# Kernel tuning notes

Hardware: AMD Instinct MI355X
Metric: run time of the kernel (lower is better)

Reference implementation:

```python
import jax, jax.numpy as jnp
import numpy as np

T, N, E = 4, 4096, 65536
XD, HD, ZD = 256, 256, 64
EPS = 1e-10


def setup_inputs() -> dict:
    key = jax.random.key(0)
    ks = jax.random.split(key, 30)
    rn = lambda k, sh, s=0.05: jax.random.normal(k, sh, dtype=jnp.float32) * s
    inp = {
        "x": rn(ks[0], (T, N, XD), 1.0),
        "edge_idx": jax.random.randint(ks[1], (T, 2, E), 0, N, dtype=jnp.int32),
        "adj": jax.random.bernoulli(ks[2], 0.005, (T, N, N)).astype(jnp.float32),
        "eps_noise": jax.random.normal(ks[3], (T, N, ZD), dtype=jnp.float32),
        "h0": jnp.zeros((1, N, HD), jnp.float32),
        # phi_x / phi_z (Linear+ReLU)
        "phi_x_w": rn(ks[4], (XD, HD)), "phi_x_b": jnp.zeros((HD,), jnp.float32),
        "phi_z_w": rn(ks[5], (ZD, HD)), "phi_z_b": jnp.zeros((HD,), jnp.float32),
        # encoder GCNs
        "enc_w": rn(ks[6], (2 * HD, HD)), "enc_b": jnp.zeros((HD,), jnp.float32),
        "enc_mean_w": rn(ks[7], (HD, ZD)), "enc_mean_b": jnp.zeros((ZD,), jnp.float32),
        "enc_std_w": rn(ks[8], (HD, ZD)), "enc_std_b": jnp.zeros((ZD,), jnp.float32),
        # prior MLPs
        "prior_w": rn(ks[9], (HD, HD)), "prior_b": jnp.zeros((HD,), jnp.float32),
        "prior_mean_w": rn(ks[10], (HD, ZD)), "prior_mean_b": jnp.zeros((ZD,), jnp.float32),
        "prior_std_w": rn(ks[11], (HD, ZD)), "prior_std_b": jnp.zeros((ZD,), jnp.float32),
        # graph-GRU GCNs (bias=False, n_layers=1; x-input is cat[phi_x, phi_z] -> 2*HD)
        "gru_xz_w": rn(ks[12], (2 * HD, HD)), "gru_hz_w": rn(ks[13], (HD, HD)),
        "gru_xr_w": rn(ks[14], (2 * HD, HD)), "gru_hr_w": rn(ks[15], (HD, HD)),
        "gru_xh_w": rn(ks[16], (2 * HD, HD)), "gru_hh_w": rn(ks[17], (HD, HD)),
    }
    return inp


def _gcn(xf, src, dst, W, b):
    """GCNConv: sym-normalized (A + I) aggregation, then bias. Returns pre-activation."""
    h = xf @ W                                             # [N, out]
    deg = 1.0 + jax.ops.segment_sum(jnp.ones(src.shape[0], xf.dtype), dst, num_segments=N)
    dinv = jax.lax.rsqrt(deg)                              # [N]
    norm = dinv[src] * dinv[dst]                           # [E]
    agg = jax.ops.segment_sum(h[src] * norm[:, None], dst, num_segments=N)
    agg = agg + (dinv * dinv)[:, None] * h                 # self-loop term
    if b is not None:
        agg = agg + b
    return agg


def reference(x, edge_idx, adj, eps_noise, h0,
              phi_x_w, phi_x_b, phi_z_w, phi_z_b,
              enc_w, enc_b, enc_mean_w, enc_mean_b, enc_std_w, enc_std_b,
              prior_w, prior_b, prior_mean_w, prior_mean_b, prior_std_w, prior_std_b,
              gru_xz_w, gru_hz_w, gru_xr_w, gru_hr_w, gru_xh_w, gru_hh_w):
    relu, sp, sig = jax.nn.relu, jax.nn.softplus, jax.nn.sigmoid
    h = h0                                                  # [1, N, HD]
    kld = jnp.float32(0.0)
    nll = jnp.float32(0.0)
    enc_means, prior_means = [], []
    nn_f = jnp.float32(N * N)
    for t in range(T):
        src, dst = edge_idx[t, 0], edge_idx[t, 1]
        phi_x_t = relu(x[t] @ phi_x_w + phi_x_b)                       # [N, HD]
        enc_in = jnp.concatenate([phi_x_t, h[-1]], axis=1)             # [N, 2HD]
        enc_t = relu(_gcn(enc_in, src, dst, enc_w, enc_b))
        enc_mean_t = _gcn(enc_t, src, dst, enc_mean_w, enc_mean_b)     # act = identity
        enc_std_t = sp(_gcn(enc_t, src, dst, enc_std_w, enc_std_b))
        prior_t = relu(h[-1] @ prior_w + prior_b)
        prior_mean_t = prior_t @ prior_mean_w + prior_mean_b
        prior_std_t = sp(prior_t @ prior_std_w + prior_std_b)
        z_t = eps_noise[t] * enc_std_t + enc_mean_t                    # reparameterize
        phi_z_t = relu(z_t @ phi_z_w + phi_z_b)
        dec_t = sig(z_t @ z_t.T)                                       # [N, N] decode
        # graph-GRU step (n_layers = 1, bias=False)
        gin = jnp.concatenate([phi_x_t, phi_z_t], axis=1)              # [N, 2HD]
        z_g = sig(_gcn(gin, src, dst, gru_xz_w, None) + _gcn(h[0], src, dst, gru_hz_w, None))
        r_g = sig(_gcn(gin, src, dst, gru_xr_w, None) + _gcn(h[0], src, dst, gru_hr_w, None))
        h_tilde = jnp.tanh(_gcn(gin, src, dst, gru_xh_w, None)
                           + _gcn(r_g * h[0], src, dst, gru_hh_w, None))
        h = (z_g * h[0] + (1.0 - z_g) * h_tilde)[None]                 # [1, N, HD]
        # KLD (faithful to _kld_gauss, including its sign convention)
        s1, s2 = enc_std_t + EPS, prior_std_t + EPS
        kld_el = (2.0 * jnp.log(s2) - 2.0 * jnp.log(s1)
                  - (s1 * s1 + (enc_mean_t - prior_mean_t) ** 2) / (s2 * s2) + 1.0)
        kld = kld + (0.5 / N) * jnp.mean(jnp.sum(kld_el, axis=0))
        # NLL (faithful quirk: BCE-with-logits applied to sigmoid output dec_t)
        a = adj[t]
        tsum = jnp.sum(a)
        posw = (nn_f - tsum) / tsum
        norm = nn_f / ((nn_f - tsum) * 2.0)
        bce = posw * a * sp(-dec_t) + (1.0 - a) * sp(dec_t)
        nll = nll + norm * jnp.mean(bce)
        enc_means.append(enc_mean_t)
        prior_means.append(prior_mean_t)
    return kld, nll, jnp.stack(enc_means), jnp.stack(prior_means), h
```

## Files before the change

### kernel.cpp

```cpp
#include <hip/hip_runtime.h>
#include <hip/hip_bf16.h>

#define T_STEPS 4
#define N 4096
#define E 65536
#define XD 256
#define HD 256
#define ZD 64

typedef __hip_bfloat16 bf16;
typedef __attribute__((ext_vector_type(8))) short short8;
typedef __attribute__((ext_vector_type(4))) float f32x4;

__device__ __forceinline__ float b2f(bf16 v){ return __bfloat162float(v); }
__device__ __forceinline__ bf16 f2b(float v){ return __float2bfloat16(v); }
__device__ __forceinline__ short f2s(float v){ return __builtin_bit_cast(short, f2b(v)); }
__device__ __forceinline__ float bits2f(unsigned int s){ return __builtin_bit_cast(float, s << 16); }
__device__ __forceinline__ float s2f(short s){ return bits2f((unsigned int)(unsigned short)s); }
__device__ __forceinline__ float splus(float x){ return (x > 20.f) ? x : log1pf(expf(x)); }
__device__ __forceinline__ float sigm(float x){ return 1.f/(1.f + expf(-x)); }

__device__ __forceinline__ float ldI(const void* p, size_t i, int f){
  return f ? ((const float*)p)[i] : b2f(((const bf16*)p)[i]);
}
__device__ __forceinline__ void stO(void* p, size_t i, float v, int f){
  if (f) ((float*)p)[i] = v; else ((bf16*)p)[i] = f2b(v);
}
__device__ __forceinline__ void ld8b(const bf16* p, float v[8]){
  uint4 u = *(const uint4*)p;
  v[0]=bits2f(u.x & 0xffffu); v[1]=bits2f(u.x >> 16);
  v[2]=bits2f(u.y & 0xffffu); v[3]=bits2f(u.y >> 16);
  v[4]=bits2f(u.z & 0xffffu); v[5]=bits2f(u.z >> 16);
  v[6]=bits2f(u.w & 0xffffu); v[7]=bits2f(u.w >> 16);
}
__device__ __forceinline__ unsigned int pack2(float a, float b){
  return (unsigned int)(unsigned short)__builtin_bit_cast(unsigned short, f2b(a))
       | ((unsigned int)(unsigned short)__builtin_bit_cast(unsigned short, f2b(b)) << 16);
}

union SMem {
  struct { short As[64*40]; short Wt[64*40]; } g;
  struct { short Zi[64*72]; short Zj[64*72]; short Adj[64*72]; float red[256]; } z;
  struct { float msh[16*128]; } m;
  int sh[256];
  float red[256];
};

struct KP {
  const void *x, *adj, *eps, *h0;
  const int* ei;
  const void *phi_x_w, *phi_x_b, *phi_z_w, *phi_z_b;
  const void *enc_w, *enc_b, *enc_mean_w, *enc_mean_b, *enc_std_w, *enc_std_b;
  const void *prior_w, *prior_b, *prior_mean_w, *prior_mean_b, *prior_std_w, *prior_std_b;
  const void *gxz, *ghz, *gxr, *ghr, *gxh, *ghh;
  void* out;
  float* scal; int* dflag; float* dinv; int* offs; int* srcs; float* enorm; int* deg;
  float* h_prev; bf16* h_bf; bf16* phiXa; bf16* Tb1; bf16* Tb2;
  bf16* zbf; float* z_g; bf16* Gs1; bf16* Gsx; bf16* Gms; bf16* Gh2;
};

#define OUT_EM ((size_t)2)
#define OUT_PM ((size_t)(2 + (size_t)T_STEPS*N*ZD))
#define OUT_H  ((size_t)(2 + (size_t)2*T_STEPS*N*ZD))

__device__ void mfma_tile(SMem& sm, int tid, int f,
    const void* A1, int am1, int lda1, const void* A2, int am2, int lda2,
    int K1, int K, const void* W, int ldw, int wcol,
    const void* bias, int act, bf16* C, int ldc, int row0, int ccol0){
  int ar = tid >> 2, akk = (tid & 3)*8;
  int wk = tid >> 3, wn = (tid & 7)*8;
  int wave = tid >> 6, lane = tid & 63, m = lane & 15, kq = lane >> 4;
  f32x4 acc[4] = {};
  for (int k0 = 0; k0 < K; k0 += 32){
    const void* A; int am, lda, kb;
    if (k0 < K1){ A = A1; am = am1; lda = lda1; kb = k0; }
    else        { A = A2; am = am2; lda = lda2; kb = k0 - K1; }
    size_t aidx = (size_t)(row0 + ar)*lda + kb + akk;
    short8 av;
    if (am == 2 || (am == 1 && f == 0)){
      av = *(const short8*)((const short*)A + aidx);
    } else {
      const float* Af = (const float*)A;
      float4 u0 = *(const float4*)(Af + aidx);
      float4 u1 = *(const float4*)(Af + aidx + 4);
      av[0]=f2s(u0.x); av[1]=f2s(u0.y); av[2]=f2s(u0.z); av[3]=f2s(u0.w);
      av[4]=f2s(u1.x); av[5]=f2s(u1.y); av[6]=f2s(u1.z); av[7]=f2s(u1.w);
    }
    *(short8*)&sm.g.As[ar*40 + akk] = av;
    size_t wi = (size_t)(k0 + wk)*ldw + wcol + wn;
    short wv[8];
    if (f == 0){
      short8 t8 = *(const short8*)((const short*)W + wi);
      #pragma unroll
      for (int j = 0; j < 8; j++) wv[j] = t8[j];
    } else {
      const float* Wf = (const float*)W;
      float4 u0 = *(const float4*)(Wf + wi);
      float4 u1 = *(const float4*)(Wf + wi + 4);
      wv[0]=f2s(u0.x); wv[1]=f2s(u0.y); wv[2]=f2s(u0.z); wv[3]=f2s(u0.w);
      wv[4]=f2s(u1.x); wv[5]=f2s(u1.y); wv[6]=f2s(u1.z); wv[7]=f2s(u1.w);
    }
    #pragma unroll
    for (int j = 0; j < 8; j++){
      int nrow = wn + j;
      int col = (((wk >> 3) ^ ((nrow >> 3) & 3)) << 3) | (wk & 7);
      sm.g.Wt[nrow*40 + col] = wv[j];
    }
    __syncthreads();
    short8 afr = *(const short8*)&sm.g.As[(wave*16 + m)*40 + kq*8];
    #pragma unroll
    for (int t4 = 0; t4 < 4; t4++){
      int nb = t4*16 + m;
      short8 bfr = *(const short8*)&sm.g.Wt[nb*40 + ((kq ^ ((nb >> 3) & 3)) << 3)];
      acc[t4] = __builtin_amdgcn_mfma_f32_16x16x32_bf16(afr, bfr, acc[t4], 0, 0, 0);
    }
    __syncthreads();
  }
  #pragma unroll
  for (int t4 = 0; t4 < 4; t4++){
    int c = ccol0 + t4*16 + m;
    float bv = bias ? ldI(bias, wcol + t4*16 + m, f) : 0.f;
    #pragma unroll
    for (int reg = 0; reg < 4; reg++){
      int r = row0 + wave*16 + kq*4 + reg;
      float v = acc[t4][reg] + bv;
      if (act == 1) v = fmaxf(v, 0.f);
      C[(size_t)r*ldc + c] = f2b(v);
    }
  }
}

__device__ void dec_tile1(const KP& p, SMem& sm, int tid, int t, int u, int f){
  int i0 = (u >> 6)*64, j0 = (u & 63)*64;
  size_t aoff = (size_t)t*N*N;
  #pragma unroll
  for (int i = 0; i < 2; i++){
    int idx = tid + i*256;
    int r = idx >> 3, c = idx & 7;
    int col = ((c ^ ((r >> 3) & 3)) << 3);
    *(short8*)&sm.z.Zi[r*72 + col] = *(const short8*)((const short*)p.zbf + (size_t)(i0+r)*ZD + c*8);
    *(short8*)&sm.z.Zj[r*72 + col] = *(const short8*)((const short*)p.zbf + (size_t)(j0+r)*ZD + c*8);
  }
  {
    int row = tid >> 2, c0 = (tid & 3)*16;
    if (f){
      const float* ap = (const float*)p.adj + aoff + (size_t)(i0+row)*N + j0 + c0;
      short tmp[16];
      #pragma unroll
      for (int q = 0; q < 16; q += 4){
        float4 v = *(const float4*)(ap + q);
        tmp[q]=f2s(v.x); tmp[q+1]=f2s(v.y); tmp[q+2]=f2s(v.z); tmp[q+3]=f2s(v.w);
      }
      *(short8*)&sm.z.Adj[row*72 + c0]     = *(short8*)&tmp[0];
      *(short8*)&sm.z.Adj[row*72 + c0 + 8] = *(short8*)&tmp[8];
    } else {
      const short* ap = (const short*)p.adj + aoff + (size_t)(i0+row)*N + j0 + c0;
      *(short8*)&sm.z.Adj[row*72 + c0]     = *(const short8*)ap;
      *(short8*)&sm.z.Adj[row*72 + c0 + 8] = *(const short8*)(ap + 8);
    }
  }
  __syncthreads();
  int wave = tid >> 6, lane = tid & 63, m = lane & 15, kq = lane >> 4;
  int ra = wave*16 + m, sa = (ra >> 3) & 3;
  short8 a1 = *(const short8*)&sm.z.Zi[ra*72 + ((kq ^ sa) << 3)];
  short8 a2 = *(const short8*)&sm.z.Zi[ra*72 + (((kq+4) ^ sa) << 3)];
  f32x4 acc[4] = {};
  #pragma unroll
  for (int t4 = 0; t4 < 4; t4++){
    int rb = t4*16 + m, sb2 = (rb >> 3) & 3;
    short8 b1 = *(const short8*)&sm.z.Zj[rb*72 + ((kq ^ sb2) << 3)];
    short8 b2 = *(const short8*)&sm.z.Zj[rb*72 + (((kq+4) ^ sb2) << 3)];
    acc[t4] = __builtin_amdgcn_mfma_f32_16x16x32_bf16(a1, b1, acc[t4], 0, 0, 0);
    acc[t4] = __builtin_amdgcn_mfma_f32_16x16x32_bf16(a2, b2, acc[t4], 0, 0, 0);
  }
  float lts = 0.f, lP = 0.f, lQ = 0.f;
  #pragma unroll
  for (int t4 = 0; t4 < 4; t4++){
    int lj = t4*16 + m;
    #pragma unroll
    for (int reg = 0; reg < 4; reg++){
      int li = wave*16 + kq*4 + reg;
      float av = s2f(sm.z.Adj[li*72 + lj]);
      float dec = sigm(acc[t4][reg]);
      lts += av;
      lQ += (1.f - av)*log1pf(expf(dec));
      if (av != 0.f) lP += av*log1pf(expf(-dec));
    }
  }
  __syncthreads();
  sm.z.red[tid] = lts; __syncthreads();
  for (int o = 128; o > 0; o >>= 1){ if (tid < o) sm.z.red[tid] += sm.z.red[tid+o]; __syncthreads(); }
  if (tid == 0) atomicAdd(p.scal + 8 + t, sm.z.red[0]);
  __syncthreads();
  sm.z.red[tid] = lP; __syncthreads();
  for (int o = 128; o > 0; o >>= 1){ if (tid < o) sm.z.red[tid] += sm.z.red[tid+o]; __syncthreads(); }
  if (tid == 0) atomicAdd(p.scal + 12 + t, sm.z.red[0]);
  __syncthreads();
  sm.z.red[tid] = lQ; __syncthreads();
  for (int o = 128; o > 0; o >>= 1){ if (tid < o) sm.z.red[tid] += sm.z.red[tid+o]; __syncthreads(); }
  if (tid == 0) atomicAdd(p.scal + 16 + t, sm.z.red[0]);
}

__global__ __launch_bounds__(256) void setup0_k(KP p){
  int gb = blockIdx.x, tid = threadIdx.x;
  if (gb == 0){ if (tid < 64) p.scal[tid] = 0.f; }
  else if (gb == 1){
    if (tid == 0){
      const unsigned short* u = (const unsigned short*)p.x;
      int big = 0;
      for (int i = 0; i < 256; i++){ int e = (u[i] >> 7) & 0xFF; if (e >= 134) big++; }
      *p.dflag = (big > 16) ? 1 : 0;
    }
  } else {
    p.deg[(gb-2)*256 + tid] = 0;
  }
}

__global__ __launch_bounds__(256) void count_deg_k(KP p){
  int idx = blockIdx.x*256 + threadIdx.x;
  int t = idx >> 16, e = idx & (E-1);
  int dst = p.ei[(size_t)t*2*E + E + e] & (N-1);
  atomicAdd(&p.deg[t*N + dst], 1);
}

__global__ __launch_bounds__(256) void setup2_k(KP p){
  __shared__ SMem sm;
  int gb = blockIdx.x, tid = threadIdx.x;
  int f = *p.dflag;
  if (gb < 4){
    int t = gb;
    const int* dg = p.deg + t*N;
    int* of = p.offs + t*(N+1);
    int base = tid*16;
    int loc[16]; int s = 0;
    #pragma unroll
    for (int i = 0; i < 16; i++){ loc[i] = s; s += dg[base+i]; }
    sm.sh[tid] = s;
    __syncthreads();
    for (int o = 1; o < 256; o <<= 1){
      int v = (tid >= o) ? sm.sh[tid-o] : 0;
      __syncthreads();
      sm.sh[tid] += v;
      __syncthreads();
    }
    int pre = (tid == 0) ? 0 : sm.sh[tid-1];
    #pragma unroll
    for (int i = 0; i < 16; i++){
      int deg_i = dg[base+i];
      of[base+i] = pre + loc[i];
      p.dinv[t*N + base + i] = rsqrtf(1.f + (float)deg_i);
    }
    if (tid == 255) of[N] = sm.sh[255];
    __syncthreads();
    #pragma unroll
    for (int i = 0; i < 16; i++) p.deg[t*N + base + i] = pre + loc[i];
  } else if (gb < 36){
    for (int idx = (gb-4)*256 + tid; idx < N*HD; idx += 32*256){
      float v = ldI(p.h0, idx, f);
      p.h_prev[idx] = v; p.h_bf[idx] = f2b(v);
    }
  } else {
    for (int u = gb - 36; u < 1024; u += 988){
      int colblk = u & 3, rowblk = u >> 2;
      mfma_tile(sm, tid, f, p.x, 1, XD, nullptr, 0, 0, XD, XD,
                p.phi_x_w, HD, colblk*64, p.phi_x_b, 1,
                p.phiXa, HD, rowblk*64, colblk*64);
    }
  }
}

__global__ __launch_bounds__(256) void scatter_k(KP p){
  int idx = blockIdx.x*256 + threadIdx.x;
  int t = idx >> 16, e = idx & (E-1);
  int s = p.ei[(size_t)t*2*E + e] & (N-1);
  int d = p.ei[(size_t)t*2*E + E + e] & (N-1);
  int pos = atomicAdd(&p.deg[t*N + d], 1);
  if (pos >= 0 && pos < E){
    p.srcs[(size_t)t*E + pos] = s;
    p.enorm[(size_t)t*E + pos] = p.dinv[t*N + s] * p.dinv[t*N + d];
  }
}

__global__ __launch_bounds__(256) void g1_k(KP p, int t){
  __shared__ SMem sm;
  int gb = blockIdx.x, tid = threadIdx.x, f = *p.dflag;
  const bf16* phiX = p.phiXa + (size_t)t*N*HD;
  int colblk = gb & 15, rowblk = gb >> 4;
  int grp = colblk >> 2, c4 = colblk & 3;
  if (grp == 0)
    mfma_tile(sm, tid, f, phiX, 2, HD, p.h_bf, 2, HD, 256, 512,
              p.enc_w, HD, c4*64, nullptr, 0, p.Gs1, 1024, rowblk*64, colblk*64);
  else if (grp == 1)
    mfma_tile(sm, tid, f, p.h_bf, 2, HD, nullptr, 0, 0, 256, 256,
              p.prior_w, HD, c4*64, p.prior_b, 1, p.Gs1, 1024, rowblk*64, colblk*64);
  else if (grp == 2)
    mfma_tile(sm, tid, f, p.h_bf, 2, HD, nullptr, 0, 0, 256, 256,
              p.ghz, HD, c4*64, nullptr, 0, p.Gs1, 1024, rowblk*64, colblk*64);
  else
    mfma_tile(sm, tid, f, p.h_bf, 2, HD, nullptr, 0, 0, 256, 256,
              p.ghr, HD, c4*64, nullptr, 0, p.Gs1, 1024, rowblk*64, colblk*64);
}

__global__ __launch_bounds__(256) void encagg_pms_k(KP p, int t){
  __shared__ SMem sm;
  int gb = blockIdx.x, tid = threadIdx.x, f = *p.dflag;
  const int* offs_t = p.offs + t*(N+1);
  const int* srcs_t = p.srcs + (size_t)t*E;
  const float* en_t = p.enorm + (size_t)t*E;
  const float* dv_t = p.dinv + t*N;
  if (gb < 512){
    int g8 = tid >> 5, l = tid & 31;
    int n = gb*8 + g8, c = l*8;
    int e0 = offs_t[n], e1 = offs_t[n+1];
    float d2 = dv_t[n]*dv_t[n];
    float acc[8], v[8];
    ld8b(p.Gs1 + (size_t)n*1024 + c, v);
    #pragma unroll
    for (int j = 0; j < 8; j++) acc[j] = d2 * v[j];
    for (int e = e0; e < e1; e++){
      int s = srcs_t[e] & (N-1);
      float nm = en_t[e];
      ld8b(p.Gs1 + (size_t)s*1024 + c, v);
      #pragma unroll
      for (int j = 0; j < 8; j++) acc[j] += nm * v[j];
    }
    #pragma unroll
    for (int j = 0; j < 8; j++) acc[j] = fmaxf(acc[j] + ldI(p.enc_b, c + j, f), 0.f);
    uint4 o; o.x = pack2(acc[0],acc[1]); o.y = pack2(acc[2],acc[3]);
    o.z = pack2(acc[4],acc[5]); o.w = pack2(acc[6],acc[7]);
    *(uint4*)(p.Tb1 + (size_t)n*HD + c) = o;
  } else {
    int u = gb - 512;
    int colblk = u & 1, rowblk = u >> 1;
    mfma_tile(sm, tid, f, p.Gs1 + 256, 2, 1024, nullptr, 0, 0, 256, 256,
              colblk ? p.prior_std_w : p.prior_mean_w, ZD, 0,
              colblk ? p.prior_std_b : p.prior_mean_b, 0,
              p.Gms, 256, rowblk*64, 128 + colblk*64);
  }
}

__global__ __launch_bounds__(256) void encms_k(KP p, int t){
  __shared__ SMem sm;
  int gb = blockIdx.x, tid = threadIdx.x, f = *p.dflag;
  int colblk = gb & 1, rowblk = gb >> 1;
  mfma_tile(sm, tid, f, p.Tb1, 2, HD, nullptr, 0, 0, 256, 256,
            colblk ? p.enc_std_w : p.enc_mean_w, ZD, 0, nullptr, 0,
            p.Gms, 256, rowblk*64, colblk*64);
}

__global__ __launch_bounds__(256) void msaggpost_k(KP p, int t){
  __shared__ SMem sm;
  int gb = blockIdx.x, tid = threadIdx.x, f = *p.dflag;
  const int* offs_t = p.offs + t*(N+1);
  const int* srcs_t = p.srcs + (size_t)t*E;
  const float* en_t = p.enorm + (size_t)t*E;
  const float* dv_t = p.dinv + t*N;
  int g16 = tid >> 4, l = tid & 15;
  int n = gb*16 + g16, c = l*8;
  {
    int e0 = offs_t[n], e1 = offs_t[n+1];
    float d2 = dv_t[n]*dv_t[n];
    float acc[8], v[8];
    ld8b(p.Gms + (size_t)n*256 + c, v);
    #pragma unroll
    for (int j = 0; j < 8; j++) acc[j] = d2 * v[j];
    for (int e = e0; e < e1; e++){
      int s = srcs_t[e] & (N-1);
      float nm = en_t[e];
      ld8b(p.Gms + (size_t)s*256 + c, v);
      #pragma unroll
      for (int j = 0; j < 8; j++) acc[j] += nm * v[j];
    }
    #pragma unroll
    for (int j = 0; j < 8; j++) sm.m.msh[g16*128 + c + j] = acc[j];
  }
  __syncthreads();
  float el = 0.f;
  {
    int d0 = l*4;
    #pragma unroll
    for (int q = 0; q < 4; q++){
      int d = d0 + q;
      size_t idx = (size_t)n*ZD + d;
      float mean = sm.m.msh[g16*128 + d] + ldI(p.enc_mean_b, d, f);
      float sd = splus(sm.m.msh[g16*128 + 64 + d] + ldI(p.enc_std_b, d, f));
      float zv = ldI(p.eps, (size_t)t*N*ZD + idx, f) * sd + mean;
      p.zbf[idx] = f2b(zv);
      stO(p.out, OUT_EM + (size_t)t*N*ZD + idx, mean, f);
      float pm = b2f(p.Gms[(size_t)n*256 + 128 + d]);
      float ps = splus(b2f(p.Gms[(size_t)n*256 + 192 + d]));
      stO(p.out, OUT_PM + (size_t)t*N*ZD + idx, pm, f);
      float s1 = sd + 1e-10f, s2 = ps + 1e-10f;
      float dm = mean - pm;
      el += 2.f*(logf(s2) - logf(s1)) - (s1*s1 + dm*dm)/(s2*s2) + 1.f;
    }
  }
  __syncthreads();
  sm.red[tid] = el; __syncthreads();
  for (int o = 128; o > 0; o >>= 1){ if (tid < o) sm.red[tid] += sm.red[tid+o]; __syncthreads(); }
  if (tid == 0) atomicAdd(p.scal + 4, sm.red[0] * (0.5f/((float)N*(float)ZD)));
}

__global__ __launch_bounds__(256) void phiz_k(KP p, int t){
  __shared__ SMem sm;
  int gb = blockIdx.x, tid = threadIdx.x, f = *p.dflag;
  int colblk = gb & 3, rowblk = gb >> 2;
  mfma_tile(sm, tid, f, p.zbf, 2, ZD, nullptr, 0, 0, ZD, ZD,
            p.phi_z_w, HD, colblk*64, p.phi_z_b, 1, p.Tb2, HD, rowblk*64, colblk*64);
}

__global__ __launch_bounds__(256) void grux_dec_k(KP p, int t){
  __shared__ SMem sm;
  int gb = blockIdx.x, tid = threadIdx.x, f = *p.dflag;
  if (gb < 768){
    const bf16* phiX = p.phiXa + (size_t)t*N*HD;
    int colblk = gb % 12, rowblk = gb / 12;
    int grp = colblk >> 2, c4 = colblk & 3;
    const void* W = (grp == 0) ? p.gxz : ((grp == 1) ? p.gxr : p.gxh);
    mfma_tile(sm, tid, f, phiX, 2, HD, p.Tb2, 2, HD, 256, 512,
              W, HD, c4*64, nullptr, 0, p.Gsx, 768, rowblk*64, colblk*64);
  } else {
    dec_tile1(p, sm, tid, t, gb - 768, f);
  }
}

__global__ __launch_bounds__(256) void zr_k(KP p, int t){
  int gb = blockIdx.x, tid = threadIdx.x;
  const int* offs_t = p.offs + t*(N+1);
  const int* srcs_t = p.srcs + (size_t)t*E;
  const float* en_t = p.enorm + (size_t)t*E;
  const float* dv_t = p.dinv + t*N;
  int g4 = tid >> 6, lane = tid & 63;
  int n = gb*4 + g4, c = lane*8;
  int e0 = offs_t[n], e1 = offs_t[n+1];
  float d2 = dv_t[n]*dv_t[n];
  float acc[8], v1[8], v2[8];
  ld8b(p.Gsx + (size_t)n*768 + c, v1);
  ld8b(p.Gs1 + 512 + (size_t)n*1024 + c, v2);
  #pragma unroll
  for (int j = 0; j < 8; j++) acc[j] = d2 * (v1[j] + v2[j]);
  for (int e = e0; e < e1; e++){
    int s = srcs_t[e] & (N-1);
    float nm = en_t[e];
    ld8b(p.Gsx + (size_t)s*768 + c, v1);
    ld8b(p.Gs1 + 512 + (size_t)s*1024 + c, v2);
    #pragma unroll
    for (int j = 0; j < 8; j++) acc[j] += nm * (v1[j] + v2[j]);
  }
  if (c < 256){
    size_t base = (size_t)n*HD + c;
    float4 o0, o1;
    o0.x = sigm(acc[0]); o0.y = sigm(acc[1]); o0.z = sigm(acc[2]); o0.w = sigm(acc[3]);
    o1.x = sigm(acc[4]); o1.y = sigm(acc[5]); o1.z = sigm(acc[6]); o1.w = sigm(acc[7]);
    *(float4*)(p.z_g + base) = o0;
    *(float4*)(p.z_g + base + 4) = o1;
  } else {
    size_t base = (size_t)n*HD + (c - 256);
    float r[8];
    #pragma unroll
    for (int j = 0; j < 8; j++) r[j] = sigm(acc[j]) * p.h_prev[base+j];
    uint4 o; o.x = pack2(r[0],r[1]); o.y = pack2(r[2],r[3]);
    o.z = pack2(r[4],r[5]); o.w = pack2(r[6],r[7]);
    *(uint4*)(p.Tb1 + base) = o;
  }
}

__global__ __launch_bounds__(256) void hh_k(KP p, int t){
  __shared__ SMem sm;
  int gb = blockIdx.x, tid = threadIdx.x, f = *p.dflag;
  int colblk = gb & 3, rowblk = gb >> 2;
  mfma_tile(sm, tid, f, p.Tb1, 2, HD, nullptr, 0, 0, 256, 256,
            p.ghh, HD, colblk*64, nullptr, 0, p.Gh2, 256, rowblk*64, colblk*64);
}

__global__ __launch_bounds__(256) void hagg_k(KP p, int t){
  int gb = blockIdx.x, tid = threadIdx.x, f = *p.dflag;
  const int* offs_t = p.offs + t*(N+1);
  const int* srcs_t = p.srcs + (size_t)t*E;
  const float* en_t = p.enorm + (size_t)t*E;
  const float* dv_t = p.dinv + t*N;
  int g8 = tid >> 5, l = tid & 31;
  int n = gb*8 + g8, c = l*8;
  int e0 = offs_t[n], e1 = offs_t[n+1];
  float d2 = dv_t[n]*dv_t[n];
  float acc[8], v1[8], v2[8];
  ld8b(p.Gsx + 512 + (size_t)n*768 + c, v1);
  ld8b(p.Gh2 + (size_t)n*256 + c, v2);
  #pragma unroll
  for (int j = 0; j < 8; j++) acc[j] = d2 * (v1[j] + v2[j]);
  for (int e = e0; e < e1; e++){
    int s = srcs_t[e] & (N-1);
    float nm = en_t[e];
    ld8b(p.Gsx + 512 + (size_t)s*768 + c, v1);
    ld8b(p.Gh2 + (size_t)s*256 + c, v2);
    #pragma unroll
    for (int j = 0; j < 8; j++) acc[j] += nm * (v1[j] + v2[j]);
  }
  size_t base = (size_t)n*HD + c;
  #pragma unroll
  for (int j = 0; j < 8; j++){
    float z = p.z_g[base+j];
    float hv = p.h_prev[base+j];
    float nv = z*hv + (1.f - z)*tanhf(acc[j]);
    p.h_prev[base+j] = nv;
    p.h_bf[base+j] = f2b(nv);
    if (t == T_STEPS-1) stO(p.out, OUT_H + base + j, nv, f);
  }
}

__global__ void fin_k(KP p){
  if (threadIdx.x == 0){
    int f = *p.dflag;
    const float NNf = 16777216.f;
    float nll = 0.f;
    for (int t = 0; t < T_STEPS; t++){
      float ts = p.scal[8+t], P = p.scal[12+t], Q = p.scal[16+t];
      float posw = (NNf - ts)/ts;
      nll += (posw*P + Q) * 0.5f/(NNf - ts);
    }
    stO(p.out, 0, p.scal[4], f);
    stO(p.out, 1, nll, f);
  }
}

extern "C" void kernel_launch(void* const* d_in, const int* in_sizes, int n_in,
                              void* d_out, int out_size, void* d_ws, size_t ws_size,
                              hipStream_t stream){
  KP P;
  P.x = d_in[0];  P.ei = (const int*)d_in[1];  P.adj = d_in[2];  P.eps = d_in[3];  P.h0 = d_in[4];
  P.phi_x_w = d_in[5];  P.phi_x_b = d_in[6];  P.phi_z_w = d_in[7];  P.phi_z_b = d_in[8];
  P.enc_w = d_in[9];  P.enc_b = d_in[10];
  P.enc_mean_w = d_in[11];  P.enc_mean_b = d_in[12];
  P.enc_std_w = d_in[13];   P.enc_std_b = d_in[14];
  P.prior_w = d_in[15];  P.prior_b = d_in[16];
  P.prior_mean_w = d_in[17];  P.prior_mean_b = d_in[18];
  P.prior_std_w = d_in[19];   P.prior_std_b = d_in[20];
  P.gxz = d_in[21];  P.ghz = d_in[22];  P.gxr = d_in[23];
  P.ghr = d_in[24];  P.gxh = d_in[25];  P.ghh = d_in[26];
  P.out = d_out;

  char* wp = (char*)d_ws;
  auto alloc = [&](size_t bytes){ void* q = (void*)wp; wp += (bytes + 255) & ~(size_t)255; return q; };
  P.scal  = (float*)alloc(64*sizeof(float));
  P.dflag = (int*)  alloc(256);
  P.dinv  = (float*)alloc((size_t)T_STEPS*N*4);
  P.offs  = (int*)  alloc((size_t)T_STEPS*(N+1)*4);
  P.srcs  = (int*)  alloc((size_t)T_STEPS*E*4);
  P.enorm = (float*)alloc((size_t)T_STEPS*E*4);
  P.deg   = (int*)  alloc((size_t)T_STEPS*N*4);
  P.h_prev= (float*)alloc((size_t)N*HD*4);
  P.h_bf  = (bf16*) alloc((size_t)N*HD*2);
  P.phiXa = (bf16*) alloc((size_t)T_STEPS*N*HD*2);
  P.Tb1   = (bf16*) alloc((size_t)N*HD*2);
  P.Tb2   = (bf16*) alloc((size_t)N*HD*2);
  P.zbf   = (bf16*) alloc((size_t)N*ZD*2);
  P.z_g   = (float*)alloc((size_t)N*HD*4);
  P.Gs1   = (bf16*) alloc((size_t)N*1024*2);
  P.Gsx   = (bf16*) alloc((size_t)N*768*2);
  P.Gms   = (bf16*) alloc((size_t)N*256*2);
  P.Gh2   = (bf16*) alloc((size_t)N*256*2);

  setup0_k<<<66,256,0,stream>>>(P);
  count_deg_k<<<1024,256,0,stream>>>(P);
  setup2_k<<<1024,256,0,stream>>>(P);
  scatter_k<<<1024,256,0,stream>>>(P);
  for (int t = 0; t < T_STEPS; t++){
    g1_k<<<1024,256,0,stream>>>(P, t);
    encagg_pms_k<<<640,256,0,stream>>>(P, t);
    encms_k<<<128,256,0,stream>>>(P, t);
    msaggpost_k<<<256,256,0,stream>>>(P, t);
    phiz_k<<<256,256,0,stream>>>(P, t);
    grux_dec_k<<<4864,256,0,stream>>>(P, t);
    zr_k<<<1024,256,0,stream>>>(P, t);
    hh_k<<<256,256,0,stream>>>(P, t);
    hagg_k<<<512,256,0,stream>>>(P, t);
  }
  fin_k<<<1,64,0,stream>>>(P);
}
```

Before: 1.546 ms.

## Fuse encoder mean/std, prior mean/std and phi_z into one aggregation kernel

The encoder mean/std GCN is reordered to aggregate the 256-wide hidden features first and then transform them. That transform is fused with the prior mean/std projection, the reparameterised z sample, the KLD reduction and the phi_z linear layer into one per-16-node kernel. These small products now use scalar FMAs with weights read from global memory instead of separate MFMA tile kernels, and the Gms intermediate buffer goes away. The final scalar write moves into an extra block of the last hagg launch, and the phi_x setup grid is widened so each block handles one tile. The aim is fewer launches and fewer round trips through global memory. The cost is a gather that is twice as wide and non-MFMA matmuls run on only 256 blocks.

Result: slower. 2.081 ms (+34.6%).

```diff
diff --git a/kernel.cpp b/kernel.cpp
--- a/kernel.cpp
+++ b/kernel.cpp
@@ -33,6 +33,14 @@
   v[4]=bits2f(u.z & 0xffffu); v[5]=bits2f(u.z >> 16);
   v[6]=bits2f(u.w & 0xffffu); v[7]=bits2f(u.w >> 16);
 }
+__device__ __forceinline__ void ldW8(const void* W, size_t off, int f, float w[8]){
+  if (f == 0){ ld8b((const bf16*)W + off, w); }
+  else {
+    const float* Wf = (const float*)W + off;
+    float4 a = *(const float4*)Wf, b = *(const float4*)(Wf + 4);
+    w[0]=a.x; w[1]=a.y; w[2]=a.z; w[3]=a.w; w[4]=b.x; w[5]=b.y; w[6]=b.z; w[7]=b.w;
+  }
+}
 __device__ __forceinline__ unsigned int pack2(float a, float b){
   return (unsigned int)(unsigned short)__builtin_bit_cast(unsigned short, f2b(a))
        | ((unsigned int)(unsigned short)__builtin_bit_cast(unsigned short, f2b(b)) << 16);
@@ -41,7 +49,6 @@
 union SMem {
   struct { short As[64*40]; short Wt[64*40]; } g;
   struct { short Zi[64*72]; short Zj[64*72]; short Adj[64*72]; float red[256]; } z;
-  struct { float msh[16*128]; } m;
   int sh[256];
   float red[256];
 };
@@ -56,7 +63,7 @@
   void* out;
   float* scal; int* dflag; float* dinv; int* offs; int* srcs; float* enorm; int* deg;
   float* h_prev; bf16* h_bf; bf16* phiXa; bf16* Tb1; bf16* Tb2;
-  bf16* zbf; float* z_g; bf16* Gs1; bf16* Gsx; bf16* Gms; bf16* Gh2;
+  bf16* zbf; float* z_g; bf16* Gs1; bf16* Gsx; bf16* Gh2;
 };
 
 #define OUT_EM ((size_t)2)
@@ -88,17 +95,15 @@
     }
     *(short8*)&sm.g.As[ar*40 + akk] = av;
     size_t wi = (size_t)(k0 + wk)*ldw + wcol + wn;
-    short wv[8];
+    float wf[8]; short wv[8];
     if (f == 0){
       short8 t8 = *(const short8*)((const short*)W + wi);
       #pragma unroll
       for (int j = 0; j < 8; j++) wv[j] = t8[j];
     } else {
-      const float* Wf = (const float*)W;
-      float4 u0 = *(const float4*)(Wf + wi);
-      float4 u1 = *(const float4*)(Wf + wi + 4);
-      wv[0]=f2s(u0.x); wv[1]=f2s(u0.y); wv[2]=f2s(u0.z); wv[3]=f2s(u0.w);
-      wv[4]=f2s(u1.x); wv[5]=f2s(u1.y); wv[6]=f2s(u1.z); wv[7]=f2s(u1.w);
+      ldW8(W, wi, f, wf);
+      #pragma unroll
+      for (int j = 0; j < 8; j++) wv[j] = f2s(wf[j]);
     }
     #pragma unroll
     for (int j = 0; j < 8; j++){
@@ -260,12 +265,11 @@
       p.h_prev[idx] = v; p.h_bf[idx] = f2b(v);
     }
   } else {
-    for (int u = gb - 36; u < 1024; u += 988){
-      int colblk = u & 3, rowblk = u >> 2;
-      mfma_tile(sm, tid, f, p.x, 1, XD, nullptr, 0, 0, XD, XD,
-                p.phi_x_w, HD, colblk*64, p.phi_x_b, 1,
-                p.phiXa, HD, rowblk*64, colblk*64);
-    }
+    int u = gb - 36;
+    int colblk = u & 3, rowblk = u >> 2;
+    mfma_tile(sm, tid, f, p.x, 1, XD, nullptr, 0, 0, XD, XD,
+              p.phi_x_w, HD, colblk*64, p.phi_x_b, 1,
+              p.phiXa, HD, rowblk*64, colblk*64);
   }
 }
 
@@ -301,78 +305,109 @@
               p.ghr, HD, c4*64, nullptr, 0, p.Gs1, 1024, rowblk*64, colblk*64);
 }
 
-__global__ __launch_bounds__(256) void encagg_pms_k(KP p, int t){
-  __shared__ SMem sm;
+__global__ __launch_bounds__(256) void encagg_k(KP p, int t){
   int gb = blockIdx.x, tid = threadIdx.x, f = *p.dflag;
   const int* offs_t = p.offs + t*(N+1);
   const int* srcs_t = p.srcs + (size_t)t*E;
   const float* en_t = p.enorm + (size_t)t*E;
   const float* dv_t = p.dinv + t*N;
-  if (gb < 512){
-    int g8 = tid >> 5, l = tid & 31;
-    int n = gb*8 + g8, c = l*8;
-    int e0 = offs_t[n], e1 = offs_t[n+1];
-    float d2 = dv_t[n]*dv_t[n];
-    float acc[8], v[8];
-    ld8b(p.Gs1 + (size_t)n*1024 + c, v);
-    #pragma unroll
-    for (int j = 0; j < 8; j++) acc[j] = d2 * v[j];
-    for (int e = e0; e < e1; e++){
-      int s = srcs_t[e] & (N-1);
-      float nm = en_t[e];
-      ld8b(p.Gs1 + (size_t)s*1024 + c, v);
-      #pragma unroll
-      for (int j = 0; j < 8; j++) acc[j] += nm * v[j];
-    }
-    #pragma unroll
-    for (int j = 0; j < 8; j++) acc[j] = fmaxf(acc[j] + ldI(p.enc_b, c + j, f), 0.f);
-    uint4 o; o.x = pack2(acc[0],acc[1]); o.y = pack2(acc[2],acc[3]);
-    o.z = pack2(acc[4],acc[5]); o.w = pack2(acc[6],acc[7]);
-    *(uint4*)(p.Tb1 + (size_t)n*HD + c) = o;
-  } else {
-    int u = gb - 512;
-    int colblk = u & 1, rowblk = u >> 1;
-    mfma_tile(sm, tid, f, p.Gs1 + 256, 2, 1024, nullptr, 0, 0, 256, 256,
-              colblk ? p.prior_std_w : p.prior_mean_w, ZD, 0,
-              colblk ? p.prior_std_b : p.prior_mean_b, 0,
-              p.Gms, 256, rowblk*64, 128 + colblk*64);
-  }
-}
-
-__global__ __launch_bounds__(256) void encms_k(KP p, int t){
-  __shared__ SMem sm;
-  int gb = blockIdx.x, tid = threadIdx.x, f = *p.dflag;
-  int colblk = gb & 1, rowblk = gb >> 1;
-  mfma_tile(sm, tid, f, p.Tb1, 2, HD, nullptr, 0, 0, 256, 256,
-            colblk ? p.enc_std_w : p.enc_mean_w, ZD, 0, nullptr, 0,
-            p.Gms, 256, rowblk*64, colblk*64);
-}
-
-__global__ __launch_bounds__(256) void msaggpost_k(KP p, int t){
-  __shared__ SMem sm;
+  int g8 = tid >> 5, l = tid & 31;
+  int n = gb*8 + g8, c = l*8;
+  int e0 = offs_t[n], e1 = offs_t[n+1];
+  float d2 = dv_t[n]*dv_t[n];
+  float acc[8], v[8];
+  ld8b(p.Gs1 + (size_t)n*1024 + c, v);
+  #pragma unroll
+  for (int j = 0; j < 8; j++) acc[j] = d2 * v[j];
+  for (int e = e0; e < e1; e++){
+    int s = srcs_t[e] & (N-1);
+    float nm = en_t[e];
+    ld8b(p.Gs1 + (size_t)s*1024 + c, v);
+    #pragma unroll
+    for (int j = 0; j < 8; j++) acc[j] += nm * v[j];
+  }
+  #pragma unroll
+  for (int j = 0; j < 8; j++) acc[j] = fmaxf(acc[j] + ldI(p.enc_b, c + j, f), 0.f);
+  uint4 o; o.x = pack2(acc[0],acc[1]); o.y = pack2(acc[2],acc[3]);
+  o.z = pack2(acc[4],acc[5]); o.w = pack2(acc[6],acc[7]);
+  *(uint4*)(p.Tb1 + (size_t)n*HD + c) = o;
+}
+
+__global__ __launch_bounds__(256) void msagg_k(KP p, int t){
+  __shared__ struct {
+    float aggT[16*260];
+    short priorT[16*264];
+    float msL[16*132];
+    float pmsL[16*132];
+    float zL[16*68];
+    float red[256];
+  } sm;
   int gb = blockIdx.x, tid = threadIdx.x, f = *p.dflag;
   const int* offs_t = p.offs + t*(N+1);
   const int* srcs_t = p.srcs + (size_t)t*E;
   const float* en_t = p.enorm + (size_t)t*E;
   const float* dv_t = p.dinv + t*N;
-  int g16 = tid >> 4, l = tid & 15;
-  int n = gb*16 + g16, c = l*8;
+  int nd = tid >> 4, l = tid & 15;
+  int n = gb*16 + nd;
   {
+    int c = l*16;
     int e0 = offs_t[n], e1 = offs_t[n+1];
     float d2 = dv_t[n]*dv_t[n];
-    float acc[8], v[8];
-    ld8b(p.Gms + (size_t)n*256 + c, v);
-    #pragma unroll
-    for (int j = 0; j < 8; j++) acc[j] = d2 * v[j];
+    float acc[16], v[8];
+    ld8b(p.Tb1 + (size_t)n*HD + c, v);
+    #pragma unroll
+    for (int j = 0; j < 8; j++) acc[j] = d2*v[j];
+    ld8b(p.Tb1 + (size_t)n*HD + c + 8, v);
+    #pragma unroll
+    for (int j = 0; j < 8; j++) acc[8+j] = d2*v[j];
     for (int e = e0; e < e1; e++){
       int s = srcs_t[e] & (N-1);
       float nm = en_t[e];
-      ld8b(p.Gms + (size_t)s*256 + c, v);
-      #pragma unroll
-      for (int j = 0; j < 8; j++) acc[j] += nm * v[j];
-    }
-    #pragma unroll
-    for (int j = 0; j < 8; j++) sm.m.msh[g16*128 + c + j] = acc[j];
+      ld8b(p.Tb1 + (size_t)s*HD + c, v);
+      #pragma unroll
+      for (int j = 0; j < 8; j++) acc[j] += nm*v[j];
+      ld8b(p.Tb1 + (size_t)s*HD + c + 8, v);
+      #pragma unroll
+      for (int j = 0; j < 8; j++) acc[8+j] += nm*v[j];
+    }
+    #pragma unroll
+    for (int j = 0; j < 16; j++) sm.aggT[nd*260 + c + j] = acc[j];
+    *(short8*)&sm.priorT[nd*264 + l*16] =
+        *(const short8*)((const short*)p.Gs1 + (size_t)n*1024 + 256 + l*16);
+    *(short8*)&sm.priorT[nd*264 + l*16 + 8] =
+        *(const short8*)((const short*)p.Gs1 + (size_t)n*1024 + 256 + l*16 + 8);
+  }
+  __syncthreads();
+  {
+    int c8 = l*8;
+    const void* W = (c8 < 64) ? p.enc_mean_w : p.enc_std_w;
+    int wc = c8 & 63;
+    float acc[8] = {};
+    #pragma unroll 4
+    for (int k = 0; k < 256; k++){
+      float a = sm.aggT[nd*260 + k];
+      float w[8]; ldW8(W, (size_t)k*ZD + wc, f, w);
+      #pragma unroll
+      for (int j = 0; j < 8; j++) acc[j] += a*w[j];
+    }
+    #pragma unroll
+    for (int j = 0; j < 8; j++) sm.msL[nd*132 + c8 + j] = acc[j];
+  }
+  {
+    int c8 = l*8;
+    const void* W = (c8 < 64) ? p.prior_mean_w : p.prior_std_w;
+    const void* B = (c8 < 64) ? p.prior_mean_b : p.prior_std_b;
+    int wc = c8 & 63;
+    float acc[8] = {};
+    #pragma unroll 4
+    for (int k = 0; k < 256; k++){
+      float a = s2f(sm.priorT[nd*264 + k]);
+      float w[8]; ldW8(W, (size_t)k*ZD + wc, f, w);
+      #pragma unroll
+      for (int j = 0; j < 8; j++) acc[j] += a*w[j];
+    }
+    #pragma unroll
+    for (int j = 0; j < 8; j++) sm.pmsL[nd*132 + c8 + j] = acc[j] + ldI(B, wc + j, f);
   }
   __syncthreads();
   float el = 0.f;
@@ -382,13 +417,14 @@
     for (int q = 0; q < 4; q++){
       int d = d0 + q;
       size_t idx = (size_t)n*ZD + d;
-      float mean = sm.m.msh[g16*128 + d] + ldI(p.enc_mean_b, d, f);
-      float sd = splus(sm.m.msh[g16*128 + 64 + d] + ldI(p.enc_std_b, d, f));
-      float zv = ldI(p.eps, (size_t)t*N*ZD + idx, f) * sd + mean;
+      float mean = sm.msL[nd*132 + d] + ldI(p.enc_mean_b, d, f);
+      float sd = splus(sm.msL[nd*132 + 64 + d] + ldI(p.enc_std_b, d, f));
+      float zv = ldI(p.eps, (size_t)t*N*ZD + idx, f)*sd + mean;
+      sm.zL[nd*68 + d] = zv;
       p.zbf[idx] = f2b(zv);
       stO(p.out, OUT_EM + (size_t)t*N*ZD + idx, mean, f);
-      float pm = b2f(p.Gms[(size_t)n*256 + 128 + d]);
-      float ps = splus(b2f(p.Gms[(size_t)n*256 + 192 + d]));
+      float pm = sm.pmsL[nd*132 + d];
+      float ps = splus(sm.pmsL[nd*132 + 64 + d]);
       stO(p.out, OUT_PM + (size_t)t*N*ZD + idx, pm, f);
       float s1 = sd + 1e-10f, s2 = ps + 1e-10f;
       float dm = mean - pm;
@@ -396,17 +432,34 @@
     }
   }
   __syncthreads();
+  {
+    int c0 = l*16;
+    float acc[16] = {};
+    #pragma unroll 4
+    for (int k = 0; k < 64; k++){
+      float zk = sm.zL[nd*68 + k];
+      float w[8];
+      ldW8(p.phi_z_w, (size_t)k*HD + c0, f, w);
+      #pragma unroll
+      for (int j = 0; j < 8; j++) acc[j] += zk*w[j];
+      ldW8(p.phi_z_w, (size_t)k*HD + c0 + 8, f, w);
+      #pragma unroll
+      for (int j = 0; j < 8; j++) acc[8+j] += zk*w[j];
+    }
+    #pragma unroll
+    for (int j = 0; j < 16; j++)
+      acc[j] = fmaxf(acc[j] + ldI(p.phi_z_b, c0 + j, f), 0.f);
+    uint4 o0, o1;
+    o0.x = pack2(acc[0],acc[1]);  o0.y = pack2(acc[2],acc[3]);
+    o0.z = pack2(acc[4],acc[5]);  o0.w = pack2(acc[6],acc[7]);
+    o1.x = pack2(acc[8],acc[9]);  o1.y = pack2(acc[10],acc[11]);
+    o1.z = pack2(acc[12],acc[13]); o1.w = pack2(acc[14],acc[15]);
+    *(uint4*)(p.Tb2 + (size_t)n*HD + c0) = o0;
+    *(uint4*)(p.Tb2 + (size_t)n*HD + c0 + 8) = o1;
+  }
   sm.red[tid] = el; __syncthreads();
   for (int o = 128; o > 0; o >>= 1){ if (tid < o) sm.red[tid] += sm.red[tid+o]; __syncthreads(); }
   if (tid == 0) atomicAdd(p.scal + 4, sm.red[0] * (0.5f/((float)N*(float)ZD)));
-}
-
-__global__ __launch_bounds__(256) void phiz_k(KP p, int t){
-  __shared__ SMem sm;
-  int gb = blockIdx.x, tid = threadIdx.x, f = *p.dflag;
-  int colblk = gb & 3, rowblk = gb >> 2;
-  mfma_tile(sm, tid, f, p.zbf, 2, ZD, nullptr, 0, 0, ZD, ZD,
-            p.phi_z_w, HD, colblk*64, p.phi_z_b, 1, p.Tb2, HD, rowblk*64, colblk*64);
 }
 
 __global__ __launch_bounds__(256) void grux_dec_k(KP p, int t){
@@ -475,6 +528,20 @@
 
 __global__ __launch_bounds__(256) void hagg_k(KP p, int t){
   int gb = blockIdx.x, tid = threadIdx.x, f = *p.dflag;
+  if (gb >= 512){
+    if (tid == 0){
+      const float NNf = 16777216.f;
+      float nll = 0.f;
+      for (int tt = 0; tt < T_STEPS; tt++){
+        float ts = p.scal[8+tt], P = p.scal[12+tt], Q = p.scal[16+tt];
+        float posw = (NNf - ts)/ts;
+        nll += (posw*P + Q) * 0.5f/(NNf - ts);
+      }
+      stO(p.out, 0, p.scal[4], f);
+      stO(p.out, 1, nll, f);
+    }
+    return;
+  }
   const int* offs_t = p.offs + t*(N+1);
   const int* srcs_t = p.srcs + (size_t)t*E;
   const float* en_t = p.enorm + (size_t)t*E;
@@ -505,21 +572,6 @@
     p.h_prev[base+j] = nv;
     p.h_bf[base+j] = f2b(nv);
     if (t == T_STEPS-1) stO(p.out, OUT_H + base + j, nv, f);
-  }
-}
-
-__global__ void fin_k(KP p){
-  if (threadIdx.x == 0){
-    int f = *p.dflag;
-    const float NNf = 16777216.f;
-    float nll = 0.f;
-    for (int t = 0; t < T_STEPS; t++){
-      float ts = p.scal[8+t], P = p.scal[12+t], Q = p.scal[16+t];
-      float posw = (NNf - ts)/ts;
-      nll += (posw*P + Q) * 0.5f/(NNf - ts);
-    }
-    stO(p.out, 0, p.scal[4], f);
-    stO(p.out, 1, nll, f);
   }
 }
 
@@ -557,23 +609,19 @@
   P.z_g   = (float*)alloc((size_t)N*HD*4);
   P.Gs1   = (bf16*) alloc((size_t)N*1024*2);
   P.Gsx   = (bf16*) alloc((size_t)N*768*2);
-  P.Gms   = (bf16*) alloc((size_t)N*256*2);
   P.Gh2   = (bf16*) alloc((size_t)N*256*2);
 
   setup0_k<<<66,256,0,stream>>>(P);
   count_deg_k<<<1024,256,0,stream>>>(P);
-  setup2_k<<<1024,256,0,stream>>>(P);
+  setup2_k<<<1060,256,0,stream>>>(P);
   scatter_k<<<1024,256,0,stream>>>(P);
   for (int t = 0; t < T_STEPS; t++){
     g1_k<<<1024,256,0,stream>>>(P, t);
-    encagg_pms_k<<<640,256,0,stream>>>(P, t);
-    encms_k<<<128,256,0,stream>>>(P, t);
-    msaggpost_k<<<256,256,0,stream>>>(P, t);
-    phiz_k<<<256,256,0,stream>>>(P, t);
+    encagg_k<<<512,256,0,stream>>>(P, t);
+    msagg_k<<<256,256,0,stream>>>(P, t);
     grux_dec_k<<<4864,256,0,stream>>>(P, t);
     zr_k<<<1024,256,0,stream>>>(P, t);
     hh_k<<<256,256,0,stream>>>(P, t);
-    hagg_k<<<512,256,0,stream>>>(P, t);
-  }
-  fin_k<<<1,64,0,stream>>>(P);
-}
+    hagg_k<<<(t == T_STEPS-1) ? 513 : 512,256,0,stream>>>(P, t);
+  }
+}
```
